# Kernel optimization log

Measured on AMD Instinct MI355X. Metric: run time of the kernel, lower is better.

## Reference

```python
import jax, jax.numpy as jnp
import numpy as np

N = 8192
IN_F = 256
OUT_F = 128
ALPHA = 0.2  # LeakyReLU negative slope
NEG = -1e12


def setup_inputs() -> dict:
    key = jax.random.key(0)
    k1, k2, k3, k4, k5, k6 = jax.random.split(key, 6)
    inp = jax.random.normal(k1, (N, IN_F), dtype=jnp.float32)
    adj = jax.random.randint(k2, (N, N), 0, 2, dtype=jnp.int32)
    # xavier_uniform with gain=1.414
    def xavier(k, shape, gain=1.414):
        fan_in, fan_out = shape[0], shape[1]
        bound = gain * np.sqrt(6.0 / (fan_in + fan_out))
        return jax.random.uniform(k, shape, jnp.float32, -bound, bound)
    W = xavier(k3, (IN_F, OUT_F))
    a = xavier(k4, (2 * OUT_F, 1))
    W_2 = xavier(k5, (IN_F, OUT_F))
    a_2 = xavier(k6, (2 * OUT_F, 1))
    return {"inp": inp, "adj": adj, "W": W, "a": a, "W_2": W_2, "a_2": a_2}


def _gat_head(h, a_vec, mask):
    # Equivalent to e[i,j] = leakyrelu(a^T [h_i ; h_j]) without N^2*2F concat:
    # split a into source/destination halves.
    a_src = a_vec[:OUT_F, 0]   # [F]
    a_dst = a_vec[OUT_F:, 0]   # [F]
    e = (h @ a_src)[:, None] + (h @ a_dst)[None, :]        # [N, N]
    e = jnp.where(e > 0, e, ALPHA * e)                      # LeakyReLU
    e = jnp.where(mask, e, NEG)
    att = jax.nn.softmax(e, axis=1)                         # [N, N]
    # dropout omitted (eval mode, training=False)
    return att @ h                                          # [N, F]


def reference(inp, adj, W, a, W_2, a_2):
    h = inp @ W      # [N, F]
    h_2 = inp @ W_2  # [N, F]
    mask = adj > 0   # adj is nonneg ints so adj*adj>0 is the same mask
    h_prime = _gat_head(h, a, mask)
    h_prime_2 = _gat_head(h_2, a_2, mask)
    h_total = h_prime + 0.5 * h_prime_2
    return jax.nn.elu(h_total)  # concat=True
```

## Files before the change

### kernel.cpp

```cpp
#include <hip/hip_runtime.h>
#include <hip/hip_fp16.h>

#define NN 8192
#define INF 256
#define OUTF 128
#define LOG2E 1.44269504088896340736f

typedef float f32x4 __attribute__((ext_vector_type(4)));
typedef float f32x16 __attribute__((ext_vector_type(16)));
typedef __fp16 h16x8 __attribute__((ext_vector_type(8)));
typedef __fp16 h16x4 __attribute__((ext_vector_type(4)));
typedef __fp16 h16x2 __attribute__((ext_vector_type(2)));
typedef int i32x4 __attribute__((ext_vector_type(4)));

__device__ __forceinline__ void gload_lds16(const void* g, void* l) {
  __builtin_amdgcn_global_load_lds(
      (const __attribute__((address_space(1))) unsigned int*)g,
      (__attribute__((address_space(3))) unsigned int*)l, 16, 0, 0);
}

__global__ __launch_bounds__(256) void kb_pack(const int* __restrict__ adj,
                                               unsigned short* __restrict__ adjb) {
  int gid = blockIdx.x * 256 + threadIdx.x;
#pragma unroll
  for (int it = 0; it < 8; ++it) {
    size_t c = (size_t)it * 524288 + gid;
    const int* p = adj + c * 16;
    i32x4 v0 = *(const i32x4*)(p);
    i32x4 v1 = *(const i32x4*)(p + 4);
    i32x4 v2 = *(const i32x4*)(p + 8);
    i32x4 v3 = *(const i32x4*)(p + 12);
    unsigned int b = 0;
#pragma unroll
    for (int k = 0; k < 4; ++k) {
      b |= (v0[k] != 0 ? 1u : 0u) << k;
      b |= (v1[k] != 0 ? 1u : 0u) << (4 + k);
      b |= (v2[k] != 0 ? 1u : 0u) << (8 + k);
      b |= (v3[k] != 0 ? 1u : 0u) << (12 + k);
    }
    adjb[c] = (unsigned short)b;
  }
}

__global__ __launch_bounds__(256) void k0_wt(const float* __restrict__ W1,
                                             const float* __restrict__ W2,
                                             __fp16* __restrict__ WT) {
  int m = blockIdx.x * 256 + threadIdx.x;
  int h = m >> 12;
  int r = m & 4095;
  int c = r >> 5;
  int kb = (r >> 1) & 15;
  int hh = r & 1;
  const float* W = h ? W2 : W1;
  float v[8];
#pragma unroll
  for (int s = 0; s < 8; ++s) {
    int koff = 4 * hh + (s & 3) + 8 * (s >> 2);
    v[s] = W[(kb * 16 + koff) * OUTF + c];
  }
  union { h16x2 h2[4]; i32x4 q; } u;
  u.h2[0] = __builtin_amdgcn_cvt_pkrtz(v[0], v[1]);
  u.h2[1] = __builtin_amdgcn_cvt_pkrtz(v[2], v[3]);
  u.h2[2] = __builtin_amdgcn_cvt_pkrtz(v[4], v[5]);
  u.h2[3] = __builtin_amdgcn_cvt_pkrtz(v[6], v[7]);
  *(i32x4*)(WT + (size_t)h * 32768 + c * 256 + kb * 16 + hh * 8) = u.q;
}

__global__ __launch_bounds__(128) void k1_h(
    const float* __restrict__ inp, const __fp16* __restrict__ WT,
    const float* __restrict__ a1, const float* __restrict__ a2,
    __fp16* __restrict__ hT2, float* __restrict__ S, float* __restrict__ D) {
  __shared__ __align__(16) float hl[2][32][136];
  int tid = threadIdx.x;
  int w = tid >> 6;
  int l = tid & 63;
  int lr = l & 31, g = l >> 5;
  int i0 = blockIdx.x * 32;
  const __fp16* WTh = WT + (size_t)w * 32768;
  f32x16 acc[4];
#pragma unroll
  for (int nf = 0; nf < 4; ++nf)
#pragma unroll
    for (int e = 0; e < 16; ++e) acc[nf][e] = 0.0f;
  const float* ip = inp + (size_t)(i0 + lr) * INF;
#pragma unroll
  for (int kb = 0; kb < 16; ++kb) {
    f32x4 q0 = *(const f32x4*)(ip + kb * 16 + 4 * g);
    f32x4 q1 = *(const f32x4*)(ip + kb * 16 + 8 + 4 * g);
    union { h16x2 h2[4]; h16x8 h8; } ua;
    ua.h2[0] = __builtin_amdgcn_cvt_pkrtz(q0[0], q0[1]);
    ua.h2[1] = __builtin_amdgcn_cvt_pkrtz(q0[2], q0[3]);
    ua.h2[2] = __builtin_amdgcn_cvt_pkrtz(q1[0], q1[1]);
    ua.h2[3] = __builtin_amdgcn_cvt_pkrtz(q1[2], q1[3]);
#pragma unroll
    for (int nf = 0; nf < 4; ++nf) {
      h16x8 b = *(const h16x8*)(WTh + (nf * 32 + lr) * 256 + kb * 16 + g * 8);
      acc[nf] = __builtin_amdgcn_mfma_f32_32x32x16_f16(ua.h8, b, acc[nf], 0, 0, 0);
    }
  }
#pragma unroll
  for (int nf = 0; nf < 4; ++nf)
#pragma unroll
    for (int r = 0; r < 16; ++r) {
      int row = (r & 3) + 8 * (r >> 2) + 4 * g;
      hl[w][row][nf * 32 + lr] = acc[nf][r];
    }
  __syncthreads();
  const float* av = w ? a2 : a1;
  float s = 0.f, d = 0.f;
#pragma unroll
  for (int cc = 0; cc < 64; cc += 4) {
    int c = g * 64 + cc;
    f32x4 hv = *(const f32x4*)&hl[w][lr][c];
    f32x4 as = *(const f32x4*)(av + c);
    f32x4 ad = *(const f32x4*)(av + 128 + c);
    s += hv[0] * as[0] + hv[1] * as[1] + hv[2] * as[2] + hv[3] * as[3];
    d += hv[0] * ad[0] + hv[1] * ad[1] + hv[2] * ad[2] + hv[3] * ad[3];
  }
  s += __shfl_xor(s, 32);
  d += __shfl_xor(d, 32);
  if (g == 0) {
    S[(size_t)w * NN + i0 + lr] = s * LOG2E;
    D[(size_t)w * NN + i0 + lr] = d * LOG2E;
  }
  __fp16* hTh = hT2 + (size_t)w * (NN * OUTF);
#pragma unroll
  for (int it = 0; it < 8; ++it) {
    int id = it * 64 + l;
    int jb = id >> 8;
    int sub = id & 255;
    int nf = sub >> 6, lq = sub & 63;
    int lqr = lq & 31, lqg = lq >> 5;
    float v[8];
#pragma unroll
    for (int s2 = 0; s2 < 8; ++s2) {
      int kloc = 4 * lqg + (s2 & 3) + 8 * (s2 >> 2);
      v[s2] = hl[w][jb * 16 + kloc][nf * 32 + lqr];
    }
    union { h16x2 h2[4]; i32x4 q; } u2;
    u2.h2[0] = __builtin_amdgcn_cvt_pkrtz(v[0], v[1]);
    u2.h2[1] = __builtin_amdgcn_cvt_pkrtz(v[2], v[3]);
    u2.h2[2] = __builtin_amdgcn_cvt_pkrtz(v[4], v[5]);
    u2.h2[3] = __builtin_amdgcn_cvt_pkrtz(v[6], v[7]);
    *(i32x4*)(hTh + (size_t)((i0 >> 4) + jb) * 2048 + sub * 8) = u2.q;
  }
}

__global__ __launch_bounds__(256) void k1c_gmax(const float* __restrict__ D,
                                                float* __restrict__ GM) {
  __shared__ float r1[256], r2[256];
  int t = threadIdx.x;
  float m1 = -1e30f, m2 = -1e30f;
  for (int i = t; i < NN; i += 256) {
    m1 = fmaxf(m1, D[i]);
    m2 = fmaxf(m2, D[NN + i]);
  }
  r1[t] = m1; r2[t] = m2;
  __syncthreads();
  for (int s = 128; s > 0; s >>= 1) {
    if (t < s) { r1[t] = fmaxf(r1[t], r1[t + s]); r2[t] = fmaxf(r2[t], r2[t + s]); }
    __syncthreads();
  }
  if (t == 0) { GM[0] = r1[0]; GM[1] = r2[0]; }
}

__global__ __launch_bounds__(256, 2) void k2_attn(
    const unsigned short* __restrict__ adjb, const __fp16* __restrict__ hT2,
    const float* __restrict__ S, const float* __restrict__ D,
    const float* __restrict__ GM, __fp16* __restrict__ NUM, float* __restrict__ DEN) {
  __shared__ __align__(16) char smem[32768];
  int tid = threadIdx.x;
  int w = tid >> 6;
  int l = tid & 63;
  int lr = l & 31, g2 = l >> 5;
  int h = w >> 1, rq = w & 1;
  int rb = blockIdx.x >> 3, js = blockIdx.x & 7;
  int i0 = rb * 128;
  int jwin = js * 1024, jw16 = js * 64;
  int base = i0 + rq * 64;
  int row0 = base + lr, row1 = base + 32 + lr;
  float gm = GM[h];
  float sf0 = S[(size_t)h * NN + row0];
  float sf1 = S[(size_t)h * NN + row1];
  float t0 = sf0 + gm, t1 = sf1 + gm;
  float cn0 = -fmaxf(t0, 0.2f * t0) - 1000.0f;
  float cn1 = -fmaxf(t1, 0.2f * t1) - 1000.0f;
  float Ac0 = sf0 + cn0, Bc0 = 0.2f * sf0 + cn0;
  float Ac1 = sf1 + cn1, Bc1 = 0.2f * sf1 + cn1;
  const float* Dh = D + (size_t)h * NN + jwin + 4 * g2;

  f32x16 acc[2][4];
#pragma unroll
  for (int f = 0; f < 2; ++f)
#pragma unroll
    for (int nf = 0; nf < 4; ++nf)
#pragma unroll
      for (int e = 0; e < 16; ++e) acc[f][nf][e] = 0.0f;
  float dsum0 = 0.f, dsum1 = 0.f;

  auto STAGE = [&](int jstep, int b) {
#pragma unroll
    for (int q = 0; q < 4; ++q) {
      int kk_l = q >> 1, hh = q & 1;
      const __fp16* gs = hT2 + (size_t)hh * (NN * OUTF) +
                         (size_t)(jw16 + jstep * 2 + kk_l) * 2048 + tid * 8;
      gload_lds16(gs, smem + b * 16384 + q * 4096 + tid * 16);
    }
  };

  const unsigned short* mrow0 = adjb + (size_t)row0 * 512 + jw16;
  const unsigned short* mrow1 = adjb + (size_t)row1 * 512 + jw16;
  i32x4 mreg0 = *(const i32x4*)(mrow0), mnext0 = *(const i32x4*)(mrow0 + 8);
  i32x4 mreg1 = *(const i32x4*)(mrow1), mnext1 = *(const i32x4*)(mrow1 + 8);

  const h16x2 ones = {(__fp16)1.0f, (__fp16)1.0f};

  STAGE(0, 0);
  __syncthreads();

  for (int j4 = 0; j4 < 8; ++j4) {
#pragma unroll
    for (int u = 0; u < 4; ++u) {
      const int jstep = j4 * 4 + u;
      const int b = jstep & 1;
      if (jstep < 31) STAGE(jstep + 1, b ^ 1);
      if (u == 0 && j4) {
        mreg0 = mnext0; mreg1 = mnext1;
        if (j4 < 7) {
          mnext0 = *(const i32x4*)(mrow0 + (j4 + 1) * 8);
          mnext1 = *(const i32x4*)(mrow1 + (j4 + 1) * 8);
        }
      }
      unsigned int dwm0 = (unsigned int)mreg0[u];
      unsigned int dwm1 = (unsigned int)mreg1[u];
#pragma unroll
      for (int kk = 0; kk < 2; ++kk) {
        int kkg = jstep * 2 + kk;
        f32x4 d0 = *(const f32x4*)(Dh + kkg * 16);
        f32x4 d1 = *(const f32x4*)(Dh + kkg * 16 + 8);
        unsigned int bts[2] = {kk ? (dwm0 >> 16) : (dwm0 & 0xffffu),
                               kk ? (dwm1 >> 16) : (dwm1 & 0xffffu)};
        h16x8 up[2];
#pragma unroll
        for (int f = 0; f < 2; ++f) {
          float Af = f ? Ac1 : Ac0, Bf_ = f ? Bc1 : Bc0;
          unsigned int bt = bts[f];
          float pv[8];
#pragma unroll
          for (int s = 0; s < 8; ++s) {
            float dd = (s < 4) ? d0[s] : d1[s - 4];
            int kloc = 4 * g2 + (s & 3) + 8 * (s >> 2);
            float uu = fmaxf(Af + dd, fmaf(0.2f, dd, Bf_));
            float bfv = (float)((bt >> kloc) & 1u);
            pv[s] = __builtin_amdgcn_exp2f(fmaf(bfv, 1000.0f, uu));
          }
          union { h16x2 h2[4]; h16x8 h8; } uq;
          uq.h2[0] = __builtin_amdgcn_cvt_pkrtz(pv[0], pv[1]);
          uq.h2[1] = __builtin_amdgcn_cvt_pkrtz(pv[2], pv[3]);
          uq.h2[2] = __builtin_amdgcn_cvt_pkrtz(pv[4], pv[5]);
          uq.h2[3] = __builtin_amdgcn_cvt_pkrtz(pv[6], pv[7]);
          float ds = f ? dsum1 : dsum0;
#if __has_builtin(__builtin_amdgcn_fdot2)
          ds = __builtin_amdgcn_fdot2(uq.h2[0], ones, ds, false);
          ds = __builtin_amdgcn_fdot2(uq.h2[1], ones, ds, false);
          ds = __builtin_amdgcn_fdot2(uq.h2[2], ones, ds, false);
          ds = __builtin_amdgcn_fdot2(uq.h2[3], ones, ds, false);
#else
          ds += ((pv[0] + pv[1]) + (pv[2] + pv[3])) + ((pv[4] + pv[5]) + (pv[6] + pv[7]));
#endif
          if (f) dsum1 = ds; else dsum0 = ds;
          up[f] = uq.h8;
        }
        const char* lb = smem + b * 16384 + (kk * 2 + h) * 4096 + l * 16;
#pragma unroll
        for (int nf = 0; nf < 4; ++nf) {
          h16x8 Bf = *(const h16x8*)(lb + nf * 1024);
          acc[0][nf] = __builtin_amdgcn_mfma_f32_32x32x16_f16(up[0], Bf, acc[0][nf], 0, 0, 0);
          acc[1][nf] = __builtin_amdgcn_mfma_f32_32x32x16_f16(up[1], Bf, acc[1][nf], 0, 0, 0);
        }
      }
      __syncthreads();
    }
  }

  dsum0 += __shfl_xor(dsum0, 32);
  dsum1 += __shfl_xor(dsum1, 32);
  if (g2 == 0) {
    DEN[(size_t)(js * 2 + h) * NN + row0] = dsum0;
    DEN[(size_t)(js * 2 + h) * NN + row1] = dsum1;
  }
#pragma unroll
  for (int f = 0; f < 2; ++f) {
    __fp16* nb = NUM + ((size_t)(js * 2 + h) * NN + base + f * 32) * 128 + lr;
#pragma unroll
    for (int nf = 0; nf < 4; ++nf)
#pragma unroll
      for (int r = 0; r < 16; ++r) {
        int crow = (r & 3) + 8 * (r >> 2) + 4 * g2;
        nb[(size_t)crow * 128 + nf * 32] = (__fp16)acc[f][nf][r];
      }
  }
}

__global__ __launch_bounds__(256) void k3_out(const __fp16* __restrict__ NUM,
                                              const float* __restrict__ DEN,
                                              float* __restrict__ out) {
  int gid = blockIdx.x * 256 + threadIdx.x;
  int i = gid >> 5;
  int c4 = (gid & 31) * 4;
  f32x4 n1 = {0.f, 0.f, 0.f, 0.f}, n2 = {0.f, 0.f, 0.f, 0.f};
  float d1 = 0.f, d2 = 0.f;
#pragma unroll
  for (int js = 0; js < 8; ++js) {
    h16x4 a1v = *(const h16x4*)(NUM + ((size_t)(js * 2 + 0) * NN + i) * 128 + c4);
    h16x4 a2v = *(const h16x4*)(NUM + ((size_t)(js * 2 + 1) * NN + i) * 128 + c4);
#pragma unroll
    for (int e = 0; e < 4; ++e) { n1[e] += (float)a1v[e]; n2[e] += (float)a2v[e]; }
    d1 += DEN[(size_t)(js * 2 + 0) * NN + i];
    d2 += DEN[(size_t)(js * 2 + 1) * NN + i];
  }
  float r1 = 1.0f / d1, r2 = 0.5f / d2;
  f32x4 o;
#pragma unroll
  for (int e = 0; e < 4; ++e) {
    float x = n1[e] * r1 + n2[e] * r2;
    o[e] = x > 0.f ? x : (exp2f(x * LOG2E) - 1.0f);
  }
  *(f32x4*)(out + (size_t)i * 128 + c4) = o;
}

extern "C" void kernel_launch(void* const* d_in, const int* in_sizes, int n_in,
                              void* d_out, int out_size, void* d_ws, size_t ws_size,
                              hipStream_t stream) {
  const float* inp = (const float*)d_in[0];
  const int* adj = (const int*)d_in[1];
  const float* W1 = (const float*)d_in[2];
  const float* a1 = (const float*)d_in[3];
  const float* W2 = (const float*)d_in[4];
  const float* a2 = (const float*)d_in[5];
  float* out = (float*)d_out;
  char* ws = (char*)d_ws;
  __fp16* WT = (__fp16*)(ws);
  __fp16* hT2 = (__fp16*)(ws + 131072);
  float* S = (float*)(ws + 4325376);
  float* D = (float*)(ws + 4390912);
  float* GM = (float*)(ws + 4456448);
  unsigned short* adjb = (unsigned short*)(ws + 4456704);
  __fp16* NUM = (__fp16*)(ws + 12845312);
  float* DEN = (float*)(ws + 46399744);

  kb_pack<<<dim3(2048), dim3(256), 0, stream>>>(adj, adjb);
  k0_wt<<<dim3(32), dim3(256), 0, stream>>>(W1, W2, WT);
  k1_h<<<dim3(256), dim3(128), 0, stream>>>(inp, WT, a1, a2, hT2, S, D);
  k1c_gmax<<<dim3(1), dim3(256), 0, stream>>>(D, GM);
  k2_attn<<<dim3(512), dim3(256), 0, stream>>>(adjb, hT2, S, D, GM, NUM, DEN);
  k3_out<<<dim3(1024), dim3(256), 0, stream>>>(NUM, DEN, out);
}
```

Before: 146.5 us.

## Software-pipeline softmax ahead of MFMA and fuse global max into projection kernel

The attention kernel now computes the masked exponentials for the next j-step into a second register set while the MFMAs for the current step run, so VALU exp work can overlap matrix-core work. Mask prefetch indices are shifted one step ahead to match. Separately, the single-block global-max kernel is removed: each wave reduces its D values and does an atomicMax on an order-preserving integer encoding, with the accumulator zeroed in the weight-transpose kernel. This removes one launch and a serial reduction, but raises register pressure in the attention kernel, which is launched with two blocks per SM.

Measured after the change: 136.8 us. -6.7%, faster.

```diff
diff --git a/kernel.cpp b/kernel.cpp
--- a/kernel.cpp
+++ b/kernel.cpp
@@ -17,6 +17,15 @@
   __builtin_amdgcn_global_load_lds(
       (const __attribute__((address_space(1))) unsigned int*)g,
       (__attribute__((address_space(3))) unsigned int*)l, 16, 0, 0);
+}
+
+__device__ __forceinline__ unsigned encf(float f) {
+  int b = __float_as_int(f);
+  return b >= 0 ? ((unsigned)b | 0x80000000u) : ~(unsigned)b;
+}
+__device__ __forceinline__ float decf(unsigned u) {
+  int b = (u & 0x80000000u) ? (int)(u & 0x7FFFFFFFu) : ~(int)u;
+  return __int_as_float(b);
 }
 
 __global__ __launch_bounds__(256) void kb_pack(const int* __restrict__ adj,
@@ -44,7 +53,9 @@
 
 __global__ __launch_bounds__(256) void k0_wt(const float* __restrict__ W1,
                                              const float* __restrict__ W2,
-                                             __fp16* __restrict__ WT) {
+                                             __fp16* __restrict__ WT,
+                                             unsigned* __restrict__ GMu) {
+  if (blockIdx.x == 0 && threadIdx.x < 2) GMu[threadIdx.x] = 0u;
   int m = blockIdx.x * 256 + threadIdx.x;
   int h = m >> 12;
   int r = m & 4095;
@@ -69,7 +80,8 @@
 __global__ __launch_bounds__(128) void k1_h(
     const float* __restrict__ inp, const __fp16* __restrict__ WT,
     const float* __restrict__ a1, const float* __restrict__ a2,
-    __fp16* __restrict__ hT2, float* __restrict__ S, float* __restrict__ D) {
+    __fp16* __restrict__ hT2, float* __restrict__ S, float* __restrict__ D,
+    unsigned* __restrict__ GMu) {
   __shared__ __align__(16) float hl[2][32][136];
   int tid = threadIdx.x;
   int w = tid >> 6;
@@ -119,10 +131,15 @@
   }
   s += __shfl_xor(s, 32);
   d += __shfl_xor(d, 32);
+  float dl = d * LOG2E;
   if (g == 0) {
     S[(size_t)w * NN + i0 + lr] = s * LOG2E;
-    D[(size_t)w * NN + i0 + lr] = d * LOG2E;
-  }
+    D[(size_t)w * NN + i0 + lr] = dl;
+  }
+  float dmax = dl;
+#pragma unroll
+  for (int off = 1; off < 32; off <<= 1) dmax = fmaxf(dmax, __shfl_xor(dmax, off));
+  if (l == 0) atomicMax(GMu + w, encf(dmax));
   __fp16* hTh = hT2 + (size_t)w * (NN * OUTF);
 #pragma unroll
   for (int it = 0; it < 8; ++it) {
@@ -146,28 +163,11 @@
   }
 }
 
-__global__ __launch_bounds__(256) void k1c_gmax(const float* __restrict__ D,
-                                                float* __restrict__ GM) {
-  __shared__ float r1[256], r2[256];
-  int t = threadIdx.x;
-  float m1 = -1e30f, m2 = -1e30f;
-  for (int i = t; i < NN; i += 256) {
-    m1 = fmaxf(m1, D[i]);
-    m2 = fmaxf(m2, D[NN + i]);
-  }
-  r1[t] = m1; r2[t] = m2;
-  __syncthreads();
-  for (int s = 128; s > 0; s >>= 1) {
-    if (t < s) { r1[t] = fmaxf(r1[t], r1[t + s]); r2[t] = fmaxf(r2[t], r2[t + s]); }
-    __syncthreads();
-  }
-  if (t == 0) { GM[0] = r1[0]; GM[1] = r2[0]; }
-}
-
 __global__ __launch_bounds__(256, 2) void k2_attn(
     const unsigned short* __restrict__ adjb, const __fp16* __restrict__ hT2,
     const float* __restrict__ S, const float* __restrict__ D,
-    const float* __restrict__ GM, __fp16* __restrict__ NUM, float* __restrict__ DEN) {
+    const unsigned* __restrict__ GMu, __fp16* __restrict__ NUM,
+    float* __restrict__ DEN) {
   __shared__ __align__(16) char smem[32768];
   int tid = threadIdx.x;
   int w = tid >> 6;
@@ -179,7 +179,7 @@
   int jwin = js * 1024, jw16 = js * 64;
   int base = i0 + rq * 64;
   int row0 = base + lr, row1 = base + 32 + lr;
-  float gm = GM[h];
+  float gm = decf(GMu[h]);
   float sf0 = S[(size_t)h * NN + row0];
   float sf1 = S[(size_t)h * NN + row1];
   float t0 = sf0 + gm, t1 = sf1 + gm;
@@ -214,8 +214,68 @@
   i32x4 mreg1 = *(const i32x4*)(mrow1), mnext1 = *(const i32x4*)(mrow1 + 8);
 
   const h16x2 ones = {(__fp16)1.0f, (__fp16)1.0f};
+  h16x8 P[2][2], Pn[2][2];
+
+  auto SOFTMAX = [&](int jn, unsigned dwm0, unsigned dwm1) {
+#pragma unroll
+    for (int kk = 0; kk < 2; ++kk) {
+      int kkg = jn * 2 + kk;
+      f32x4 d0 = *(const f32x4*)(Dh + kkg * 16);
+      f32x4 d1 = *(const f32x4*)(Dh + kkg * 16 + 8);
+      unsigned bts[2] = {kk ? (dwm0 >> 16) : (dwm0 & 0xffffu),
+                         kk ? (dwm1 >> 16) : (dwm1 & 0xffffu)};
+#pragma unroll
+      for (int f = 0; f < 2; ++f) {
+        float Af = f ? Ac1 : Ac0, Bf_ = f ? Bc1 : Bc0;
+        unsigned bt = bts[f];
+        float pv[8];
+#pragma unroll
+        for (int s = 0; s < 8; ++s) {
+          float dd = (s < 4) ? d0[s] : d1[s - 4];
+          int kloc = 4 * g2 + (s & 3) + 8 * (s >> 2);
+          float uu = fmaxf(Af + dd, fmaf(0.2f, dd, Bf_));
+          float bfv = (float)((bt >> kloc) & 1u);
+          pv[s] = __builtin_amdgcn_exp2f(fmaf(bfv, 1000.0f, uu));
+        }
+        union { h16x2 h2[4]; h16x8 h8; } uq;
+        uq.h2[0] = __builtin_amdgcn_cvt_pkrtz(pv[0], pv[1]);
+        uq.h2[1] = __builtin_amdgcn_cvt_pkrtz(pv[2], pv[3]);
+        uq.h2[2] = __builtin_amdgcn_cvt_pkrtz(pv[4], pv[5]);
+        uq.h2[3] = __builtin_amdgcn_cvt_pkrtz(pv[6], pv[7]);
+        float ds = f ? dsum1 : dsum0;
+#if __has_builtin(__builtin_amdgcn_fdot2)
+        ds = __builtin_amdgcn_fdot2(uq.h2[0], ones, ds, false);
+        ds = __builtin_amdgcn_fdot2(uq.h2[1], ones, ds, false);
+        ds = __builtin_amdgcn_fdot2(uq.h2[2], ones, ds, false);
+        ds = __builtin_amdgcn_fdot2(uq.h2[3], ones, ds, false);
+#else
+        ds += ((pv[0] + pv[1]) + (pv[2] + pv[3])) + ((pv[4] + pv[5]) + (pv[6] + pv[7]));
+#endif
+        if (f) dsum1 = ds; else dsum0 = ds;
+        Pn[f][kk] = uq.h8;
+      }
+    }
+  };
+
+  auto MFMA_STEP = [&](int b) {
+#pragma unroll
+    for (int kk = 0; kk < 2; ++kk) {
+      const char* lb = smem + b * 16384 + (kk * 2 + h) * 4096 + l * 16;
+#pragma unroll
+      for (int nf = 0; nf < 4; ++nf) {
+        h16x8 Bf = *(const h16x8*)(lb + nf * 1024);
+        acc[0][nf] = __builtin_amdgcn_mfma_f32_32x32x16_f16(P[0][kk], Bf, acc[0][nf], 0, 0, 0);
+        acc[1][nf] = __builtin_amdgcn_mfma_f32_32x32x16_f16(P[1][kk], Bf, acc[1][nf], 0, 0, 0);
+      }
+    }
+  };
 
   STAGE(0, 0);
+  SOFTMAX(0, (unsigned)mreg0[0], (unsigned)mreg1[0]);
+#pragma unroll
+  for (int f = 0; f < 2; ++f)
+#pragma unroll
+    for (int kk = 0; kk < 2; ++kk) P[f][kk] = Pn[f][kk];
   __syncthreads();
 
   for (int j4 = 0; j4 < 8; ++j4) {
@@ -224,60 +284,23 @@
       const int jstep = j4 * 4 + u;
       const int b = jstep & 1;
       if (jstep < 31) STAGE(jstep + 1, b ^ 1);
-      if (u == 0 && j4) {
+      if (u == 3) {
         mreg0 = mnext0; mreg1 = mnext1;
-        if (j4 < 7) {
-          mnext0 = *(const i32x4*)(mrow0 + (j4 + 1) * 8);
-          mnext1 = *(const i32x4*)(mrow1 + (j4 + 1) * 8);
+        if (j4 < 6) {
+          mnext0 = *(const i32x4*)(mrow0 + (j4 + 2) * 8);
+          mnext1 = *(const i32x4*)(mrow1 + (j4 + 2) * 8);
         }
       }
-      unsigned int dwm0 = (unsigned int)mreg0[u];
-      unsigned int dwm1 = (unsigned int)mreg1[u];
-#pragma unroll
-      for (int kk = 0; kk < 2; ++kk) {
-        int kkg = jstep * 2 + kk;
-        f32x4 d0 = *(const f32x4*)(Dh + kkg * 16);
-        f32x4 d1 = *(const f32x4*)(Dh + kkg * 16 + 8);
-        unsigned int bts[2] = {kk ? (dwm0 >> 16) : (dwm0 & 0xffffu),
-                               kk ? (dwm1 >> 16) : (dwm1 & 0xffffu)};
-        h16x8 up[2];
-#pragma unroll
-        for (int f = 0; f < 2; ++f) {
-          float Af = f ? Ac1 : Ac0, Bf_ = f ? Bc1 : Bc0;
-          unsigned int bt = bts[f];
-          float pv[8];
-#pragma unroll
-          for (int s = 0; s < 8; ++s) {
-            float dd = (s < 4) ? d0[s] : d1[s - 4];
-            int kloc = 4 * g2 + (s & 3) + 8 * (s >> 2);
-            float uu = fmaxf(Af + dd, fmaf(0.2f, dd, Bf_));
-            float bfv = (float)((bt >> kloc) & 1u);
-            pv[s] = __builtin_amdgcn_exp2f(fmaf(bfv, 1000.0f, uu));
-          }
-          union { h16x2 h2[4]; h16x8 h8; } uq;
-          uq.h2[0] = __builtin_amdgcn_cvt_pkrtz(pv[0], pv[1]);
-          uq.h2[1] = __builtin_amdgcn_cvt_pkrtz(pv[2], pv[3]);
-          uq.h2[2] = __builtin_amdgcn_cvt_pkrtz(pv[4], pv[5]);
-          uq.h2[3] = __builtin_amdgcn_cvt_pkrtz(pv[6], pv[7]);
-          float ds = f ? dsum1 : dsum0;
-#if __has_builtin(__builtin_amdgcn_fdot2)
-          ds = __builtin_amdgcn_fdot2(uq.h2[0], ones, ds, false);
-          ds = __builtin_amdgcn_fdot2(uq.h2[1], ones, ds, false);
-          ds = __builtin_amdgcn_fdot2(uq.h2[2], ones, ds, false);
-          ds = __builtin_amdgcn_fdot2(uq.h2[3], ones, ds, false);
-#else
-          ds += ((pv[0] + pv[1]) + (pv[2] + pv[3])) + ((pv[4] + pv[5]) + (pv[6] + pv[7]));
-#endif
-          if (f) dsum1 = ds; else dsum0 = ds;
-          up[f] = uq.h8;
-        }
-        const char* lb = smem + b * 16384 + (kk * 2 + h) * 4096 + l * 16;
-#pragma unroll
-        for (int nf = 0; nf < 4; ++nf) {
-          h16x8 Bf = *(const h16x8*)(lb + nf * 1024);
-          acc[0][nf] = __builtin_amdgcn_mfma_f32_32x32x16_f16(up[0], Bf, acc[0][nf], 0, 0, 0);
-          acc[1][nf] = __builtin_amdgcn_mfma_f32_32x32x16_f16(up[1], Bf, acc[1][nf], 0, 0, 0);
-        }
+      if (jstep < 31) {
+        const int un = (u + 1) & 3;
+        SOFTMAX(jstep + 1, (unsigned)mreg0[un], (unsigned)mreg1[un]);
+      }
+      MFMA_STEP(b);
+      if (jstep < 31) {
+#pragma unroll
+        for (int f = 0; f < 2; ++f)
+#pragma unroll
+          for (int kk = 0; kk < 2; ++kk) P[f][kk] = Pn[f][kk];
       }
       __syncthreads();
     }
@@ -344,15 +367,14 @@
   __fp16* hT2 = (__fp16*)(ws + 131072);
   float* S = (float*)(ws + 4325376);
   float* D = (float*)(ws + 4390912);
-  float* GM = (float*)(ws + 4456448);
+  unsigned* GMu = (unsigned*)(ws + 4456448);
   unsigned short* adjb = (unsigned short*)(ws + 4456704);
   __fp16* NUM = (__fp16*)(ws + 12845312);
   float* DEN = (float*)(ws + 46399744);
 
   kb_pack<<<dim3(2048), dim3(256), 0, stream>>>(adj, adjb);
-  k0_wt<<<dim3(32), dim3(256), 0, stream>>>(W1, W2, WT);
-  k1_h<<<dim3(256), dim3(128), 0, stream>>>(inp, WT, a1, a2, hT2, S, D);
-  k1c_gmax<<<dim3(1), dim3(256), 0, stream>>>(D, GM);
-  k2_attn<<<dim3(512), dim3(256), 0, stream>>>(adjb, hT2, S, D, GM, NUM, DEN);
+  k0_wt<<<dim3(32), dim3(256), 0, stream>>>(W1, W2, WT, GMu);
+  k1_h<<<dim3(256), dim3(128), 0, stream>>>(inp, WT, a1, a2, hT2, S, D, GMu);
+  k2_attn<<<dim3(512), dim3(256), 0, stream>>>(adjb, hT2, S, D, GMu, NUM, DEN);
   k3_out<<<dim3(1024), dim3(256), 0, stream>>>(NUM, DEN, out);
 }
```
